# Optimization experiments

Measured on AMD Instinct MI355X. Metric: run time of the kernel, lower is better.

Reference implementation:

```python
import jax, jax.numpy as jnp
import numpy as np

SIGNAL_LEN = 2048
N_WAVELETS = 32
TWO_PI = 2.0 * np.pi


def _encoder(x, W1, b1, W2, b2, W3, b3, W4, b4):
    B = x.shape[0]
    h = x.reshape(B, -1)                      # (B, 4096)
    h = jax.nn.relu(h @ W1.T + b1)            # (B, 1024)
    h = jax.nn.relu(h @ W2.T + b2)            # (B, 512)
    h = jax.nn.relu(h @ W3.T + b3)            # (B, 256)
    return h @ W4.T + b4                      # (B, n_wavelets*5)


def _synthesize(params):
    # params: (B, N_WAVELETS, 5)
    A = params[..., 0]                                    # (B, N)
    t0 = jax.nn.sigmoid(params[..., 1]) * SIGNAL_LEN      # (B, N)
    f = jax.nn.sigmoid(params[..., 2]) * 0.5              # (B, N)
    sigma = jax.nn.sigmoid(params[..., 3]) * 200.0 + 2.0  # (B, N)
    phi = params[..., 4]                                  # (B, N)

    t = jnp.arange(SIGNAL_LEN, dtype=params.dtype)        # (T,)
    dt = t[None, None, :] - t0[..., None]                 # (B, N, T)
    g = (A[..., None]
         * jnp.exp(-(dt * dt) / (2.0 * sigma[..., None] ** 2))
         * jnp.cos(TWO_PI * f[..., None] * dt + phi[..., None]))  # (B, N, T)
    sig = jnp.sum(g, axis=1)                              # (B, T)
    # both channels receive the identical wavelet sum (as in the torch code)
    return jnp.stack([sig, sig], axis=1)                  # (B, 2, T)


def setup_inputs() -> dict:
    key = jax.random.key(0)
    ks = jax.random.split(key, 9)
    B = 4096
    def w(k, shape, fan_in):
        return jax.random.normal(k, shape, dtype=jnp.float32) / np.sqrt(fan_in)
    return {
        "x": jax.random.normal(ks[0], (B, 2, SIGNAL_LEN), dtype=jnp.float32),
        "W1": w(ks[1], (1024, 4096), 4096), "b1": jnp.zeros((1024,), jnp.float32),
        "W2": w(ks[2], (512, 1024), 1024),  "b2": jnp.zeros((512,), jnp.float32),
        "W3": w(ks[3], (256, 512), 512),    "b3": jnp.zeros((256,), jnp.float32),
        "W4": w(ks[4], (N_WAVELETS * 5, 256), 256), "b4": jnp.zeros((N_WAVELETS * 5,), jnp.float32),
    }


def reference(x, W1, b1, W2, b2, W3, b3, W4, b4):
    B = x.shape[0]
    params = _encoder(x, W1, b1, W2, b2, W3, b3, W4, b4).reshape(B, N_WAVELETS, 5)
    return _synthesize(params)  # (B, 2, SIGNAL_LEN)
```

## Files before the change

### kernel.cpp

```cpp
#include <hip/hip_runtime.h>


#define SIGNAL_LEN 2048
#define NWAV 32

typedef _Float16 f16x8 __attribute__((ext_vector_type(8)));
typedef _Float16 f16x4 __attribute__((ext_vector_type(4)));
typedef float    f32x4 __attribute__((ext_vector_type(4)));

__device__ __forceinline__ void load16_lds(const _Float16* g, _Float16* l) {
  __builtin_amdgcn_global_load_lds((const __attribute__((address_space(1))) void*)g,
                                   (__attribute__((address_space(3))) void*)l,
                                   16, 0, 0);
}

struct HL { _Float16 h, l; };
__device__ __forceinline__ HL split_one(float a) {
  HL r;
  r.h = (_Float16)a;
  r.l = (_Float16)((a - (float)r.h) * 4096.0f);
  return r;
}

__global__ void split_x(const float4* __restrict__ src, f16x4* __restrict__ dh,
                        f16x4* __restrict__ dl) {
  int i = blockIdx.x * 256 + threadIdx.x;
  float4 v = src[i];
  float a[4] = {v.x, v.y, v.z, v.w};
  f16x4 h, l;
#pragma unroll
  for (int j = 0; j < 4; j++) {
    HL r = split_one(a[j]);
    h[j] = r.h;
    l[j] = r.l;
  }
  dh[i] = h;
  dl[i] = l;
}

__global__ void split_weights(const float* __restrict__ W1, const float* __restrict__ W2,
                              const float* __restrict__ W3, const float* __restrict__ W4,
                              const float* __restrict__ b4,
                              f16x4* __restrict__ W1h, f16x4* __restrict__ W1l,
                              f16x4* __restrict__ W2h, f16x4* __restrict__ W2l,
                              f16x4* __restrict__ W3h, f16x4* __restrict__ W3l,
                              f16x4* __restrict__ W4h, f16x4* __restrict__ W4l,
                              float* __restrict__ b4p) {
  const int blk = blockIdx.x;
  const int tid = threadIdx.x;
  if (blk < 4736) {
    const float4* src;
    f16x4 *dh, *dl;
    int i;
    if (blk < 4096) {
      src = (const float4*)W1; dh = W1h; dl = W1l; i = blk * 256 + tid;
    } else if (blk < 4608) {
      src = (const float4*)W2; dh = W2h; dl = W2l; i = (blk - 4096) * 256 + tid;
    } else {
      src = (const float4*)W3; dh = W3h; dl = W3l; i = (blk - 4608) * 256 + tid;
    }
    float4 v = src[i];
    float a[4] = {v.x * 256.0f, v.y * 256.0f, v.z * 256.0f, v.w * 256.0f};
    f16x4 h, l;
#pragma unroll
    for (int j = 0; j < 4; j++) {
      HL r = split_one(a[j]);
      h[j] = r.h;
      l[j] = r.l;
    }
    dh[i] = h;
    dl[i] = l;
  } else if (blk < 4800) {
    int i = (blk - 4736) * 256 + tid;
    int i4 = i << 2;
    int row = i4 >> 8;
    f16x4 h, l;
#pragma unroll
    for (int j = 0; j < 4; j++) {
      float a = (row < 160) ? W4[i4 + j] * 256.0f : 0.0f;
      HL r = split_one(a);
      h[j] = r.h;
      l[j] = r.l;
    }
    W4h[i] = h;
    W4l[i] = l;
  } else {
    b4p[tid] = (tid < 160) ? b4[tid] : 0.0f;
  }
}

template <int TM, int TN, int N, int K, bool RELU, bool SPLIT_OUT>
__global__ void __launch_bounds__(256, 2)
gemm_fused(const _Float16* __restrict__ Ah, const _Float16* __restrict__ Al,
           const _Float16* __restrict__ Bh, const _Float16* __restrict__ Bl,
           const float* __restrict__ bias,
           _Float16* __restrict__ Ch, _Float16* __restrict__ Cl,
           float* __restrict__ Cf) {
  constexpr int AM = TM / 32;
  constexpr int BN = TN / 32;
  constexpr int AU = TM / 8;
  constexpr int TU = (TM + TN) / 8;
  constexpr int UPW = TU / 4;
  constexpr int NK = K / 32;

  __shared__ __align__(16) _Float16 s[2][(TM + TN) * 64];

  const int tid = threadIdx.x;
  const int lane = tid & 63;
  const int w = tid >> 6;
  const int wm = w >> 1, wn = w & 1;
  const int m0 = blockIdx.y * TM;
  const int n0 = blockIdx.x * TN;

  const int srow = lane >> 2;
  const int sk8 = (((lane & 3) - (lane >> 3)) & 3) * 8;

  const _Float16* gb[UPW];
  int lo[UPW];
#pragma unroll
  for (int i = 0; i < UPW; ++i) {
    const int u = w * UPW + i;
    if (u < AU) {
      const int g = u >> 1, hl = u & 1;
      gb[i] = (hl ? Al : Ah) + (size_t)(m0 + g * 16 + srow) * K + sk8;
    } else {
      const int ub = u - AU;
      const int g = ub >> 1, hl = ub & 1;
      gb[i] = (hl ? Bl : Bh) + (size_t)(n0 + g * 16 + srow) * K + sk8;
    }
    lo[i] = u * 512;
  }

  const int fr = lane & 15;
  const int fq = lane >> 4;
  const int fslot8 = (4 * fr + ((fq + (fr >> 1)) & 3)) * 8;

  f32x4 acc1[AM][BN], acc2[AM][BN];
#pragma unroll
  for (int i = 0; i < AM; i++)
#pragma unroll
    for (int j = 0; j < BN; j++) {
      acc1[i][j] = 0.0f;
      acc2[i][j] = 0.0f;
    }

#pragma unroll
  for (int i = 0; i < UPW; ++i) load16_lds(gb[i], &s[0][lo[i]]);

  for (int kt = 0; kt < NK; ++kt) {
    const int cur = kt & 1;
    __syncthreads();

    if (kt + 1 < NK) {
      const int kofs = (kt + 1) * 32;
#pragma unroll
      for (int i = 0; i < UPW; ++i) load16_lds(gb[i] + kofs, &s[cur ^ 1][lo[i]]);
    }

    f16x8 fAh[AM], fAl[AM], fBh[BN], fBl[BN];
#pragma unroll
    for (int im = 0; im < AM; ++im) {
      const int g = wm * AM + im;
      fAh[im] = *(const f16x8*)(&s[cur][(g * 2 + 0) * 512 + fslot8]);
      fAl[im] = *(const f16x8*)(&s[cur][(g * 2 + 1) * 512 + fslot8]);
    }
#pragma unroll
    for (int in = 0; in < BN; ++in) {
      const int g = wn * BN + in;
      fBh[in] = *(const f16x8*)(&s[cur][TM * 64 + (g * 2 + 0) * 512 + fslot8]);
      fBl[in] = *(const f16x8*)(&s[cur][TM * 64 + (g * 2 + 1) * 512 + fslot8]);
    }
#pragma unroll
    for (int im = 0; im < AM; ++im) {
#pragma unroll
      for (int in = 0; in < BN; ++in) {
        acc1[im][in] = __builtin_amdgcn_mfma_f32_16x16x32_f16(fAh[im], fBh[in], acc1[im][in], 0, 0, 0);
        acc2[im][in] = __builtin_amdgcn_mfma_f32_16x16x32_f16(fAh[im], fBl[in], acc2[im][in], 0, 0, 0);
        acc2[im][in] = __builtin_amdgcn_mfma_f32_16x16x32_f16(fAl[im], fBh[in], acc2[im][in], 0, 0, 0);
      }
    }
  }

  const int quad = lane >> 4;
#pragma unroll
  for (int in = 0; in < BN; ++in) {
    const int n = n0 + wn * (TN / 2) + in * 16 + fr;
    const float bv = bias[n];
#pragma unroll
    for (int im = 0; im < AM; ++im) {
#pragma unroll
      for (int r = 0; r < 4; ++r) {
        const int m = m0 + wm * (TM / 2) + im * 16 + quad * 4 + r;
        float c = (acc1[im][in][r] + acc2[im][in][r] * (1.0f / 4096.0f)) * (1.0f / 256.0f) + bv;
        if (RELU) c = fmaxf(c, 0.0f);
        const size_t off = (size_t)m * N + n;
        if (SPLIT_OUT) {
          HL rr = split_one(c);
          Ch[off] = rr.h;
          Cl[off] = rr.l;
        } else {
          Cf[off] = c;
        }
      }
    }
  }
}

template <int TM, int TN, int N, int K, int KSPLIT, int MINW>
__global__ void __launch_bounds__(256, MINW)
gemm_part(const _Float16* __restrict__ Ah, const _Float16* __restrict__ Al,
          const _Float16* __restrict__ Bh, const _Float16* __restrict__ Bl,
          float* __restrict__ Cp) {
  constexpr int AM = TM / 32;
  constexpr int BN = TN / 32;
  constexpr int AU = TM / 8;
  constexpr int TU = (TM + TN) / 8;
  constexpr int UPW = TU / 4;
  constexpr int NK = K / KSPLIT / 32;

  __shared__ __align__(16) _Float16 s[2][(TM + TN) * 64];

  const int tid = threadIdx.x;
  const int lane = tid & 63;
  const int w = tid >> 6;
  const int wm = w >> 1, wn = w & 1;
  const int m0 = blockIdx.y * TM;
  const int n0 = blockIdx.x * TN;
  const int kb = blockIdx.z * (K / KSPLIT);

  const int srow = lane >> 2;
  const int sk8 = (((lane & 3) - (lane >> 3)) & 3) * 8;

  const _Float16* gb[UPW];
  int lo[UPW];
#pragma unroll
  for (int i = 0; i < UPW; ++i) {
    const int u = w * UPW + i;
    if (u < AU) {
      const int g = u >> 1, hl = u & 1;
      gb[i] = (hl ? Al : Ah) + (size_t)(m0 + g * 16 + srow) * K + kb + sk8;
    } else {
      const int ub = u - AU;
      const int g = ub >> 1, hl = ub & 1;
      gb[i] = (hl ? Bl : Bh) + (size_t)(n0 + g * 16 + srow) * K + kb + sk8;
    }
    lo[i] = u * 512;
  }

  const int fr = lane & 15;
  const int fq = lane >> 4;
  const int fslot8 = (4 * fr + ((fq + (fr >> 1)) & 3)) * 8;

  f32x4 acc1[AM][BN], acc2[AM][BN];
#pragma unroll
  for (int i = 0; i < AM; i++)
#pragma unroll
    for (int j = 0; j < BN; j++) {
      acc1[i][j] = 0.0f;
      acc2[i][j] = 0.0f;
    }

#pragma unroll
  for (int i = 0; i < UPW; ++i) load16_lds(gb[i], &s[0][lo[i]]);

  for (int kt = 0; kt < NK; ++kt) {
    const int cur = kt & 1;
    __syncthreads();

    if (kt + 1 < NK) {
      const int kofs = (kt + 1) * 32;
#pragma unroll
      for (int i = 0; i < UPW; ++i) load16_lds(gb[i] + kofs, &s[cur ^ 1][lo[i]]);
    }

    f16x8 fAh[AM], fAl[AM], fBh[BN], fBl[BN];
#pragma unroll
    for (int im = 0; im < AM; ++im) {
      const int g = wm * AM + im;
      fAh[im] = *(const f16x8*)(&s[cur][(g * 2 + 0) * 512 + fslot8]);
      fAl[im] = *(const f16x8*)(&s[cur][(g * 2 + 1) * 512 + fslot8]);
    }
#pragma unroll
    for (int in = 0; in < BN; ++in) {
      const int g = wn * BN + in;
      fBh[in] = *(const f16x8*)(&s[cur][TM * 64 + (g * 2 + 0) * 512 + fslot8]);
      fBl[in] = *(const f16x8*)(&s[cur][TM * 64 + (g * 2 + 1) * 512 + fslot8]);
    }
#pragma unroll
    for (int im = 0; im < AM; ++im) {
#pragma unroll
      for (int in = 0; in < BN; ++in) {
        acc1[im][in] = __builtin_amdgcn_mfma_f32_16x16x32_f16(fAh[im], fBh[in], acc1[im][in], 0, 0, 0);
        acc2[im][in] = __builtin_amdgcn_mfma_f32_16x16x32_f16(fAh[im], fBl[in], acc2[im][in], 0, 0, 0);
        acc2[im][in] = __builtin_amdgcn_mfma_f32_16x16x32_f16(fAl[im], fBh[in], acc2[im][in], 0, 0, 0);
      }
    }
  }

  const int quad = lane >> 4;
  float* Cz = Cp + (size_t)blockIdx.z * ((size_t)gridDim.y * TM) * N;
#pragma unroll
  for (int in = 0; in < BN; ++in) {
    const int n = n0 + wn * (TN / 2) + in * 16 + fr;
#pragma unroll
    for (int im = 0; im < AM; ++im) {
#pragma unroll
      for (int r = 0; r < 4; ++r) {
        const int m = m0 + wm * (TM / 2) + im * 16 + quad * 4 + r;
        Cz[(size_t)m * N + n] = acc1[im][in][r] + acc2[im][in][r] * (1.0f / 4096.0f);
      }
    }
  }
}

__global__ void __launch_bounds__(256)
combine1(const float* __restrict__ Cp, const float* __restrict__ bias, int N,
         size_t halfN, _Float16* __restrict__ Ch, _Float16* __restrict__ Cl) {
  const size_t i4 = ((size_t)blockIdx.x * 256 + threadIdx.x) * 4;
  float4 p0 = *(const float4*)(Cp + i4);
  float4 p1 = *(const float4*)(Cp + halfN + i4);
  float4 bv = *(const float4*)(bias + (i4 % (size_t)N));
  float c[4] = {(p0.x + p1.x) * (1.0f / 256.0f) + bv.x,
                (p0.y + p1.y) * (1.0f / 256.0f) + bv.y,
                (p0.z + p1.z) * (1.0f / 256.0f) + bv.z,
                (p0.w + p1.w) * (1.0f / 256.0f) + bv.w};
  f16x4 h, l;
#pragma unroll
  for (int j = 0; j < 4; j++) {
    c[j] = fmaxf(c[j], 0.0f);
    HL r = split_one(c[j]);
    h[j] = r.h;
    l[j] = r.l;
  }
  *(f16x4*)(Ch + i4) = h;
  *(f16x4*)(Cl + i4) = l;
}

__global__ void __launch_bounds__(256)
synth(const float* __restrict__ P, float* __restrict__ out) {
  __shared__ float sA[NWAV], sT0[NWAV], sF[NWAV], sC[NWAV], sPh[NWAV], sSg[NWAV];
  const int b = blockIdx.x;
  const int tid = threadIdx.x;
  if (tid < NWAV) {
    const float* q = P + (size_t)b * 256 + tid * 5;
    const float L2E = 1.44269504088896340736f;
    float A = q[0], p1 = q[1], p2 = q[2], p3 = q[3], p4 = q[4];
    float s1 = 1.0f / (1.0f + exp2f(-p1 * L2E));
    float s2 = 1.0f / (1.0f + exp2f(-p2 * L2E));
    float s3 = 1.0f / (1.0f + exp2f(-p3 * L2E));
    float sg = s3 * 200.0f + 2.0f;
    sA[tid] = A;
    sT0[tid] = s1 * 2048.0f;
    sF[tid] = s2 * 0.5f;
    sC[tid] = -L2E / (2.0f * sg * sg);
    sPh[tid] = p4 * 0.15915494309189535f;
    sSg[tid] = sg;
  }
  __syncthreads();

  const float t0f = (float)(tid * 8);
  const int wlo = (tid & ~63) * 8;
  float acc[8];
#pragma unroll
  for (int i = 0; i < 8; i++) acc[i] = 0.0f;

  for (int wv = 0; wv < NWAV; wv++) {
    const float t0 = sT0[wv], sg = sSg[wv];
    if (t0 + 5.0f * sg < (float)wlo || t0 - 5.0f * sg > (float)(wlo + 511)) continue;
    const float A = sA[wv], fr = sF[wv], cn = sC[wv], ph = sPh[wv];
#pragma unroll
    for (int i = 0; i < 8; i++) {
      float dt = (t0f + (float)i) - t0;
      float e = exp2f(dt * dt * cn);
      float r = fr * dt + ph;
      r -= floorf(r);
      float cs = __builtin_amdgcn_cosf(r);
      acc[i] += A * e * cs;
    }
  }

  float* o = out + (size_t)b * (2 * SIGNAL_LEN) + tid * 8;
  float4 v0 = make_float4(acc[0], acc[1], acc[2], acc[3]);
  float4 v1 = make_float4(acc[4], acc[5], acc[6], acc[7]);
  *(float4*)(o) = v0;
  *(float4*)(o + 4) = v1;
  *(float4*)(o + SIGNAL_LEN) = v0;
  *(float4*)(o + SIGNAL_LEN + 4) = v1;
}

extern "C" void kernel_launch(void* const* d_in, const int* in_sizes, int n_in,
                              void* d_out, int out_size, void* d_ws, size_t ws_size,
                              hipStream_t stream) {
  (void)in_sizes; (void)n_in; (void)out_size; (void)ws_size;
  const float* X  = (const float*)d_in[0];
  const float* W1 = (const float*)d_in[1];
  const float* b1 = (const float*)d_in[2];
  const float* W2 = (const float*)d_in[3];
  const float* b2 = (const float*)d_in[4];
  const float* W3 = (const float*)d_in[5];
  const float* b3 = (const float*)d_in[6];
  const float* W4 = (const float*)d_in[7];
  const float* b4 = (const float*)d_in[8];
  float* out = (float*)d_out;

  char* p = (char*)d_ws;
  auto take = [&](size_t bytes) -> char* {
    char* r = p;
    p += (bytes + 255) & ~(size_t)255;
    return r;
  };
  _Float16* Xh  = (_Float16*)take((size_t)4096 * 4096 * 2);
  _Float16* Xl  = (_Float16*)take((size_t)4096 * 4096 * 2);
  _Float16* W1h = (_Float16*)take((size_t)1024 * 4096 * 2);
  _Float16* W1l = (_Float16*)take((size_t)1024 * 4096 * 2);
  _Float16* H1h = (_Float16*)take((size_t)4096 * 1024 * 2);
  _Float16* H1l = (_Float16*)take((size_t)4096 * 1024 * 2);
  _Float16* W2h = (_Float16*)take((size_t)512 * 1024 * 2);
  _Float16* W2l = (_Float16*)take((size_t)512 * 1024 * 2);
  _Float16* H2h = (_Float16*)take((size_t)4096 * 512 * 2);
  _Float16* H2l = (_Float16*)take((size_t)4096 * 512 * 2);
  _Float16* W3h = (_Float16*)take((size_t)256 * 512 * 2);
  _Float16* W3l = (_Float16*)take((size_t)256 * 512 * 2);
  _Float16* H3h = (_Float16*)take((size_t)4096 * 256 * 2);
  _Float16* H3l = (_Float16*)take((size_t)4096 * 256 * 2);
  _Float16* W4h = (_Float16*)take((size_t)256 * 256 * 2);
  _Float16* W4l = (_Float16*)take((size_t)256 * 256 * 2);
  float*    b4p = (float*)take(256 * 4);
  float*    Pp  = (float*)take((size_t)4096 * 256 * 4);
  float*    Cp  = (float*)take((size_t)2 * 4096 * 1024 * 4);

  split_x<<<16384, 256, 0, stream>>>((const float4*)X, (f16x4*)Xh, (f16x4*)Xl);
  split_weights<<<4801, 256, 0, stream>>>(W1, W2, W3, W4, b4,
                                          (f16x4*)W1h, (f16x4*)W1l, (f16x4*)W2h, (f16x4*)W2l,
                                          (f16x4*)W3h, (f16x4*)W3l, (f16x4*)W4h, (f16x4*)W4l, b4p);

  gemm_part<128, 256, 1024, 4096, 2, 1><<<dim3(4, 32, 2), 256, 0, stream>>>(
      Xh, Xl, W1h, W1l, Cp);
  combine1<<<4096, 256, 0, stream>>>(Cp, b1, 1024, (size_t)4096 * 1024, H1h, H1l);

  gemm_fused<64, 64, 512, 1024, true, true><<<dim3(8, 64), 256, 0, stream>>>(
      H1h, H1l, W2h, W2l, b2, H2h, H2l, nullptr);
  gemm_fused<32, 64, 256, 512, true, true><<<dim3(4, 128), 256, 0, stream>>>(
      H2h, H2l, W3h, W3l, b3, H3h, H3l, nullptr);
  gemm_fused<32, 64, 256, 256, false, false><<<dim3(4, 128), 256, 0, stream>>>(
      H3h, H3l, W4h, W4l, b4p, nullptr, nullptr, Pp);

  synth<<<4096, 256, 0, stream>>>(Pp, out);
}
```

Baseline: 395.5 us.

## Rework first GEMM as 512-thread triple-buffered pipeline with finer waitcnt sync

New measurement: 458.2 us. 1.16x slower.

```diff
diff --git a/kernel.cpp b/kernel.cpp
--- a/kernel.cpp
+++ b/kernel.cpp
@@ -206,24 +206,57 @@
   }
 }
 
-template <int TM, int TN, int N, int K, int KSPLIT, int MINW>
-__global__ void __launch_bounds__(256, MINW)
-gemm_part(const _Float16* __restrict__ Ah, const _Float16* __restrict__ Al,
-          const _Float16* __restrict__ Bh, const _Float16* __restrict__ Bl,
-          float* __restrict__ Cp) {
-  constexpr int AM = TM / 32;
-  constexpr int BN = TN / 32;
+#define G1_STEP(BUF, WAITN)                                                    \
+  {                                                                            \
+    asm volatile("s_waitcnt vmcnt(" #WAITN ")" ::: "memory");                  \
+    __builtin_amdgcn_s_barrier();                                              \
+    if (kt + 2 < NK) {                                                         \
+      const int kofs = (kt + 2) * 32;                                          \
+      _Float16* dst = s3 + (((BUF) + 2) % 3) * BUFH;                           \
+      _Pragma("unroll") for (int i = 0; i < UPW; ++i)                          \
+          load16_lds(gb[i] + kofs, dst + lo[i]);                               \
+    }                                                                          \
+    const _Float16* sb = s3 + (BUF) * BUFH;                                    \
+    f16x8 fBh[BNv], fBl[BNv];                                                  \
+    _Pragma("unroll") for (int in = 0; in < BNv; ++in) {                       \
+      fBh[in] = *(const f16x8*)(sb + boff + in * 1024);                        \
+      fBl[in] = *(const f16x8*)(sb + boff + in * 1024 + 512);                  \
+    }                                                                          \
+    _Pragma("unroll") for (int im = 0; im < AMv; ++im) {                       \
+      f16x8 fAh = *(const f16x8*)(sb + aoff + im * 1024);                      \
+      f16x8 fAl = *(const f16x8*)(sb + aoff + im * 1024 + 512);                \
+      _Pragma("unroll") for (int in = 0; in < BNv; ++in) {                     \
+        acc1[im][in] = __builtin_amdgcn_mfma_f32_16x16x32_f16(fAh, fBh[in], acc1[im][in], 0, 0, 0); \
+        acc2[im][in] = __builtin_amdgcn_mfma_f32_16x16x32_f16(fAh, fBl[in], acc2[im][in], 0, 0, 0); \
+        acc2[im][in] = __builtin_amdgcn_mfma_f32_16x16x32_f16(fAl, fBh[in], acc2[im][in], 0, 0, 0); \
+      }                                                                        \
+    }                                                                          \
+    ++kt;                                                                      \
+  }
+
+template <int TM, int TN, int N, int K, int KSPLIT>
+__global__ void __launch_bounds__(512, 2)
+gemm_g1_tb(const _Float16* __restrict__ Ah, const _Float16* __restrict__ Al,
+           const _Float16* __restrict__ Bh, const _Float16* __restrict__ Bl,
+           float* __restrict__ Cp) {
+  constexpr int WTM = TM / 2;
+  constexpr int WTN = TN / 4;
+  constexpr int AMv = WTM / 16;
+  constexpr int BNv = WTN / 16;
   constexpr int AU = TM / 8;
   constexpr int TU = (TM + TN) / 8;
-  constexpr int UPW = TU / 4;
+  constexpr int UPW = TU / 8;
   constexpr int NK = K / KSPLIT / 32;
-
-  __shared__ __align__(16) _Float16 s[2][(TM + TN) * 64];
+  constexpr int BUFH = TU * 512;
+  static_assert((NK - 1) % 3 == 0, "K-loop x3 tiling requires NK = 3m+1");
+
+  __shared__ __align__(16) _Float16 s3[3 * BUFH];
 
   const int tid = threadIdx.x;
   const int lane = tid & 63;
   const int w = tid >> 6;
-  const int wm = w >> 1, wn = w & 1;
+  const int wm = w >> 2;
+  const int wn = w & 3;
   const int m0 = blockIdx.y * TM;
   const int n0 = blockIdx.x * TN;
   const int kb = blockIdx.z * (K / KSPLIT);
@@ -251,62 +284,42 @@
   const int fq = lane >> 4;
   const int fslot8 = (4 * fr + ((fq + (fr >> 1)) & 3)) * 8;
 
-  f32x4 acc1[AM][BN], acc2[AM][BN];
-#pragma unroll
-  for (int i = 0; i < AM; i++)
-#pragma unroll
-    for (int j = 0; j < BN; j++) {
+  const int aoff = wm * (AMv * 1024) + fslot8;
+  const int boff = AU * 512 + wn * (BNv * 1024) + fslot8;
+
+  f32x4 acc1[AMv][BNv], acc2[AMv][BNv];
+#pragma unroll
+  for (int i = 0; i < AMv; i++)
+#pragma unroll
+    for (int j = 0; j < BNv; j++) {
       acc1[i][j] = 0.0f;
       acc2[i][j] = 0.0f;
     }
 
 #pragma unroll
-  for (int i = 0; i < UPW; ++i) load16_lds(gb[i], &s[0][lo[i]]);
-
-  for (int kt = 0; kt < NK; ++kt) {
-    const int cur = kt & 1;
-    __syncthreads();
-
-    if (kt + 1 < NK) {
-      const int kofs = (kt + 1) * 32;
-#pragma unroll
-      for (int i = 0; i < UPW; ++i) load16_lds(gb[i] + kofs, &s[cur ^ 1][lo[i]]);
-    }
-
-    f16x8 fAh[AM], fAl[AM], fBh[BN], fBl[BN];
-#pragma unroll
-    for (int im = 0; im < AM; ++im) {
-      const int g = wm * AM + im;
-      fAh[im] = *(const f16x8*)(&s[cur][(g * 2 + 0) * 512 + fslot8]);
-      fAl[im] = *(const f16x8*)(&s[cur][(g * 2 + 1) * 512 + fslot8]);
-    }
-#pragma unroll
-    for (int in = 0; in < BN; ++in) {
-      const int g = wn * BN + in;
-      fBh[in] = *(const f16x8*)(&s[cur][TM * 64 + (g * 2 + 0) * 512 + fslot8]);
-      fBl[in] = *(const f16x8*)(&s[cur][TM * 64 + (g * 2 + 1) * 512 + fslot8]);
-    }
-#pragma unroll
-    for (int im = 0; im < AM; ++im) {
-#pragma unroll
-      for (int in = 0; in < BN; ++in) {
-        acc1[im][in] = __builtin_amdgcn_mfma_f32_16x16x32_f16(fAh[im], fBh[in], acc1[im][in], 0, 0, 0);
-        acc2[im][in] = __builtin_amdgcn_mfma_f32_16x16x32_f16(fAh[im], fBl[in], acc2[im][in], 0, 0, 0);
-        acc2[im][in] = __builtin_amdgcn_mfma_f32_16x16x32_f16(fAl[im], fBh[in], acc2[im][in], 0, 0, 0);
-      }
-    }
-  }
+  for (int i = 0; i < UPW; ++i) load16_lds(gb[i], s3 + lo[i]);
+#pragma unroll
+  for (int i = 0; i < UPW; ++i) load16_lds(gb[i] + 32, s3 + BUFH + lo[i]);
+
+  int kt = 0;
+#pragma unroll 1
+  for (int j = 0; j < (NK - 1) / 3; ++j) {
+    G1_STEP(0, 6)
+    G1_STEP(1, 6)
+    G1_STEP(2, 6)
+  }
+  G1_STEP(0, 0)
 
   const int quad = lane >> 4;
   float* Cz = Cp + (size_t)blockIdx.z * ((size_t)gridDim.y * TM) * N;
 #pragma unroll
-  for (int in = 0; in < BN; ++in) {
-    const int n = n0 + wn * (TN / 2) + in * 16 + fr;
-#pragma unroll
-    for (int im = 0; im < AM; ++im) {
+  for (int in = 0; in < BNv; ++in) {
+    const int n = n0 + wn * WTN + in * 16 + fr;
+#pragma unroll
+    for (int im = 0; im < AMv; ++im) {
 #pragma unroll
       for (int r = 0; r < 4; ++r) {
-        const int m = m0 + wm * (TM / 2) + im * 16 + quad * 4 + r;
+        const int m = m0 + wm * WTM + im * 16 + quad * 4 + r;
         Cz[(size_t)m * N + n] = acc1[im][in][r] + acc2[im][in][r] * (1.0f / 4096.0f);
       }
     }
@@ -434,7 +447,7 @@
                                           (f16x4*)W1h, (f16x4*)W1l, (f16x4*)W2h, (f16x4*)W2l,
                                           (f16x4*)W3h, (f16x4*)W3l, (f16x4*)W4h, (f16x4*)W4l, b4p);
 
-  gemm_part<128, 256, 1024, 4096, 2, 1><<<dim3(4, 32, 2), 256, 0, stream>>>(
+  gemm_g1_tb<128, 256, 1024, 4096, 2><<<dim3(4, 32, 2), 512, 0, stream>>>(
       Xh, Xl, W1h, W1l, Cp);
   combine1<<<4096, 256, 0, stream>>>(Cp, b1, 1024, (size_t)4096 * 1024, H1h, H1l);
 
```
